# Kernel optimization log

Hardware: AMD Instinct MI355X
Metric: run time of the kernel (lower is better)

## Reference

```python
import jax, jax.numpy as jnp
import numpy as np

B, F, V, D, K = 16384, 39, 30000, 16, 20
EPS = 1e-5


def bn_eval(x, g, b):
    # inference-mode BatchNorm1d with running_mean=0, running_var=1
    return g * x / jnp.sqrt(1.0 + EPS) + b


def setup_inputs() -> dict:
    key = jax.random.key(0)
    ks = jax.random.split(key, 12)
    x = jax.random.randint(ks[0], (B, F), 0, V)
    emb_table = jax.random.normal(ks[1], (F * V, D), dtype=jnp.float32) * 0.05
    w_c = jax.random.normal(ks[2], (F, F * D), dtype=jnp.float32) * 0.05
    w0 = jax.random.normal(ks[3], (1024, F * D), dtype=jnp.float32) * 0.04
    w1 = jax.random.normal(ks[4], (512, 1024), dtype=jnp.float32) * 0.03
    w_out = jax.random.normal(ks[5], (1, 512), dtype=jnp.float32) * 0.04
    return {
        'x': x, 'emb_table': emb_table,
        'w_c': w_c, 'b_c': jnp.zeros((F,)), 'g_c': jnp.ones((F,)), 'be_c': jnp.zeros((F,)),
        'w0': w0, 'b0': jnp.zeros((1024,)), 'g0': jnp.ones((1024,)), 'be0': jnp.zeros((1024,)),
        'w1': w1, 'b1': jnp.zeros((512,)), 'g1': jnp.ones((512,)), 'be1': jnp.zeros((512,)),
        'w_out': w_out, 'b_out': jnp.zeros((1,)),
    }


def reference(x, emb_table, w_c, b_c, g_c, be_c, w0, b0, g0, be0,
              w1, b1, g1, be1, w_out, b_out):
    offsets = jnp.arange(F, dtype=x.dtype) * V          # per-field offsets
    idx = x + offsets[None, :]                          # [B, F]
    emb = emb_table[idx]                                # [B, F, D] gather

    # controller_mlp: flatten (batch, D, F) layout like torch transpose(1,2)
    flat = jnp.transpose(emb, (0, 2, 1)).reshape(B, F * D)
    h = jax.nn.relu(bn_eval(flat @ w_c.T + b_c, g_c, be_c))
    scores = jax.nn.softmax(h, axis=1)                  # [B, F]

    # kmax_pooling: top-k field indices, sorted ascending, gather weights
    _, kidx = jax.lax.top_k(scores, K)
    kidx = jnp.sort(kidx, axis=1)                       # [B, K]
    w = jnp.take_along_axis(scores, kidx, axis=1)       # [B, K]

    # forward_select: gather selected field embeddings, weight them
    sel = jnp.take_along_axis(emb, kidx[:, :, None], axis=1)  # [B, K, D]
    weighted = sel * w[:, :, None]

    # scatter back into full field slots (unselected fields are zero)
    full = jnp.zeros((B, F, D), weighted.dtype)
    bidx = jnp.arange(B)[:, None]
    full = full.at[bidx, kidx].set(weighted)            # [B, F, D]

    z = jnp.transpose(full, (0, 2, 1)).reshape(B, F * D)
    z = jax.nn.relu(bn_eval(z @ w0.T + b0, g0, be0))
    z = jax.nn.relu(bn_eval(z @ w1.T + b1, g1, be1))
    out = jax.nn.sigmoid(z @ w_out.T + b_out)           # [B, 1]
    return out.squeeze(-1)
```

## Files before the change

### kernel.cpp

```cpp
#include <hip/hip_runtime.h>
#include <math.h>

#define B_SZ 16384
#define F_N 39
#define V_N 30000
#define D_N 16
#define K_SEL 20
#define FD 624
#define KP0 640
#define NCP 48
#define N0 1024
#define N1 512
#define CBR 16
#define ALD 648

typedef unsigned short u16;
typedef __attribute__((ext_vector_type(8))) short bf16x8;
typedef __attribute__((ext_vector_type(8))) unsigned short u16x8;
typedef __attribute__((ext_vector_type(4))) float f32x4;
typedef __attribute__((ext_vector_type(4))) unsigned short u16x4;

__device__ __forceinline__ u16 f2bf(float v) {
    union { float f; unsigned u; } x; x.f = v;
    unsigned r = x.u + 0x7fff + ((x.u >> 16) & 1);
    return (u16)(r >> 16);
}
__device__ __forceinline__ float bf2f(u16 v) {
    union { unsigned u; float f; } x; x.u = ((unsigned)v) << 16;
    return x.f;
}

#define GLD16(gp, lp) __builtin_amdgcn_global_load_lds( \
    (const __attribute__((address_space(1))) unsigned int*)(gp), \
    (__attribute__((address_space(3))) unsigned int*)(lp), 16, 0, 0)

#define PREP_W0 (N0 * KP0)
#define PREP_W1 (N1 * N0)
#define PREP_WC (NCP * KP0)
#define PREP_TOT (PREP_W0 + PREP_W1 + PREP_WC + 3 * NCP)

__global__ __launch_bounds__(256) void prep_all_kernel(
    const float* __restrict__ w0, const float* __restrict__ w1,
    const float* __restrict__ w_c, const float* __restrict__ b_c,
    const float* __restrict__ g_c, const float* __restrict__ be_c,
    u16* __restrict__ w0b, u16* __restrict__ w1b, u16* __restrict__ wcb,
    float* __restrict__ bcp, float* __restrict__ gcp, float* __restrict__ becp)
{
    int i = blockIdx.x * blockDim.x + threadIdx.x;
    if (i < PREP_W0) {
        int n = i / KP0, kk = i - n * KP0;
        float v = 0.f;
        if (kk < FD) v = w0[n * FD + (kk & 15) * F_N + (kk >> 4)];
        w0b[i] = f2bf(v);
        return;
    }
    i -= PREP_W0;
    if (i < PREP_W1) { w1b[i] = f2bf(w1[i]); return; }
    i -= PREP_W1;
    if (i < PREP_WC) {
        int n = i / KP0, kk = i - n * KP0;
        float v = 0.f;
        if (n < F_N && kk < FD) v = w_c[n * FD + (kk & 15) * F_N + (kk >> 4)];
        wcb[i] = f2bf(v);
        return;
    }
    i -= PREP_WC;
    if (i < 3 * NCP) {
        int which = i / NCP, n = i - which * NCP;
        float v = 0.f;
        if (n < F_N) v = (which == 0) ? b_c[n] : (which == 1) ? g_c[n] : be_c[n];
        ((which == 0) ? bcp : (which == 1) ? gcp : becp)[n] = v;
    }
}

__global__ __launch_bounds__(256) void fused_controller_kernel(
    const int* __restrict__ x, const float* __restrict__ emb_table,
    const u16* __restrict__ wcb, const float* __restrict__ bcp,
    const float* __restrict__ gcp, const float* __restrict__ becp,
    u16* __restrict__ zb)
{
    __shared__ __align__(16) u16 Al[CBR * ALD];
    __shared__ float vv[CBR][49];
    __shared__ f32x4 part[4][64][3];
    __shared__ float selw[CBR][F_N];

    const int t    = threadIdx.x;
    const int wave = t >> 6;
    const int lane = t & 63;
    const int b0   = blockIdx.x * CBR;

    for (int p = t; p < CBR * F_N; p += 256) {
        const int row = p / F_N;
        const int f   = p - row * F_N;
        const int xi  = x[b0 * F_N + p];
        const float4* src = (const float4*)(emb_table + (size_t)(xi + f * V_N) * D_N);
        float4 v0 = src[0], v1 = src[1], v2 = src[2], v3 = src[3];
        u16x8 o0 = { f2bf(v0.x), f2bf(v0.y), f2bf(v0.z), f2bf(v0.w),
                     f2bf(v1.x), f2bf(v1.y), f2bf(v1.z), f2bf(v1.w) };
        u16x8 o1 = { f2bf(v2.x), f2bf(v2.y), f2bf(v2.z), f2bf(v2.w),
                     f2bf(v3.x), f2bf(v3.y), f2bf(v3.z), f2bf(v3.w) };
        *(u16x8*)&Al[row * ALD + f * D_N]     = o0;
        *(u16x8*)&Al[row * ALD + f * D_N + 8] = o1;
    }
    __syncthreads();

    const int m = lane & 15;
    const int q = lane >> 4;
    f32x4 acc0 = {}, acc1 = {}, acc2 = {};
    {
        const u16* ap  = &Al[m * ALD + wave * 160 + q * 8];
        const u16* bp0 = wcb + (size_t)(0  + m) * KP0 + wave * 160 + q * 8;
        const u16* bp1 = wcb + (size_t)(16 + m) * KP0 + wave * 160 + q * 8;
        const u16* bp2 = wcb + (size_t)(32 + m) * KP0 + wave * 160 + q * 8;
        #pragma unroll
        for (int k = 0; k < 5; ++k) {
            bf16x8 af = *(const bf16x8*)ap;
            bf16x8 b0 = *(const bf16x8*)bp0;
            bf16x8 b1 = *(const bf16x8*)bp1;
            bf16x8 b2 = *(const bf16x8*)bp2;
            acc0 = __builtin_amdgcn_mfma_f32_16x16x32_bf16(af, b0, acc0, 0, 0, 0);
            acc1 = __builtin_amdgcn_mfma_f32_16x16x32_bf16(af, b1, acc1, 0, 0, 0);
            acc2 = __builtin_amdgcn_mfma_f32_16x16x32_bf16(af, b2, acc2, 0, 0, 0);
            ap += 32; bp0 += 32; bp1 += 32; bp2 += 32;
        }
    }
    part[wave][lane][0] = acc0;
    part[wave][lane][1] = acc1;
    part[wave][lane][2] = acc2;
    __syncthreads();

    if (wave == 0) {
        f32x4 r0 = part[0][lane][0] + part[1][lane][0] + part[2][lane][0] + part[3][lane][0];
        f32x4 r1 = part[0][lane][1] + part[1][lane][1] + part[2][lane][1] + part[3][lane][1];
        f32x4 r2 = part[0][lane][2] + part[1][lane][2] + part[2][lane][2] + part[3][lane][2];

        const float rs = rsqrtf(1.0f + 1e-5f);
        #pragma unroll
        for (int j = 0; j < 3; ++j) {
            const f32x4 a = (j == 0) ? r0 : (j == 1) ? r1 : r2;
            const int n = j * 16 + m;
            const float gn = gcp[n] * rs;
            const float bn = becp[n];
            const float bi = bcp[n];
            #pragma unroll
            for (int r = 0; r < 4; ++r)
                vv[q * 4 + r][n] = fmaxf(fmaf(gn, a[r] + bi, bn), 0.f);
        }

        const int row = lane >> 2;
        const int fg  = lane & 3;
        float e[10];
        float mloc = -1e30f;
        #pragma unroll
        for (int it = 0; it < 10; ++it) {
            const int f = fg + 4 * it;
            if (f < F_N) { e[it] = vv[row][f]; mloc = fmaxf(mloc, e[it]); }
        }
        mloc = fmaxf(mloc, __shfl_xor(mloc, 1, 64));
        mloc = fmaxf(mloc, __shfl_xor(mloc, 2, 64));
        float sloc = 0.f;
        #pragma unroll
        for (int it = 0; it < 10; ++it) {
            const int f = fg + 4 * it;
            if (f < F_N) { e[it] = expf(e[it] - mloc); sloc += e[it]; }
        }
        sloc += __shfl_xor(sloc, 1, 64);
        sloc += __shfl_xor(sloc, 2, 64);
        const float inv = 1.f / sloc;
        #pragma unroll
        for (int it = 0; it < 10; ++it) {
            const int f = fg + 4 * it;
            if (f < F_N) vv[row][f] = e[it];
        }

        int rank[10] = {};
        for (int gg = 0; gg < F_N; ++gg) {
            const float o = vv[row][gg];
            #pragma unroll
            for (int it = 0; it < 10; ++it) {
                const int f = fg + 4 * it;
                if (f < F_N)
                    rank[it] += (o > e[it] || (o == e[it] && gg < f)) ? 1 : 0;
            }
        }
        #pragma unroll
        for (int it = 0; it < 10; ++it) {
            const int f = fg + 4 * it;
            if (f < F_N)
                selw[row][f] = (rank[it] < K_SEL) ? e[it] * inv : 0.f;
        }
    }
    __syncthreads();

    for (int gp = t; gp < CBR * 40; gp += 256) {
        const int row  = gp & 15;
        const int slot = gp >> 4;
        u16* dst = zb + (size_t)(b0 + row) * KP0 + slot * D_N;
        u16x8 o0 = {0,0,0,0,0,0,0,0}, o1 = {0,0,0,0,0,0,0,0};
        if (slot < F_N) {
            const float w = selw[row][slot];
            u16x8 a0 = *(u16x8*)&Al[row * ALD + slot * D_N];
            u16x8 a1 = *(u16x8*)&Al[row * ALD + slot * D_N + 8];
            #pragma unroll
            for (int k = 0; k < 8; ++k) {
                o0[k] = f2bf(bf2f(a0[k]) * w);
                o1[k] = f2bf(bf2f(a1[k]) * w);
            }
        }
        *(u16x8*)dst = o0;
        *(u16x8*)(dst + 8) = o1;
    }
}

template<int MODE>
__global__ __launch_bounds__(256) void gemm_mfma_bn_relu(
    const u16* __restrict__ A, const u16* __restrict__ W,
    const float* __restrict__ bias, const float* __restrict__ g,
    const float* __restrict__ be, u16* __restrict__ Cout,
    int M, int N, int Kp,
    const float* __restrict__ w_out, float* __restrict__ outp)
{
    __shared__ __align__(16) u16 As[128 * 32];
    __shared__ __align__(16) u16 Bs[128 * 32];

    const int t    = threadIdx.x;
    const int wave = t >> 6;
    const int lane = t & 63;
    const int wm   = wave >> 1, wn = wave & 1;
    const int m0   = blockIdx.x * 128;
    const int n0   = blockIdx.y * 128;

    const int lr    = lane >> 2;
    const int swz_u = (lane & 3) ^ ((lane >> 3) & 3);
    const u16* gA0 = A + (size_t)(m0 + wave * 32 + lr) * Kp + swz_u * 8;
    const u16* gA1 = gA0 + 16 * (size_t)Kp;
    const u16* gB0 = W + (size_t)(n0 + wave * 32 + lr) * Kp + swz_u * 8;
    const u16* gB1 = gB0 + 16 * (size_t)Kp;
    u16* lA0 = &As[(wave * 32)      * 32];
    u16* lA1 = &As[(wave * 32 + 16) * 32];
    u16* lB0 = &Bs[(wave * 32)      * 32];
    u16* lB1 = &Bs[(wave * 32 + 16) * 32];

    const int q    = lane >> 4;
    const int lr16 = lane & 15;

    int aoff[4], boff[4];
    #pragma unroll
    for (int i = 0; i < 4; ++i) {
        int ra = wm * 64 + i * 16 + lr16;
        aoff[i] = ra * 32 + ((q ^ ((ra >> 1) & 3)) * 8);
        int rb = wn * 64 + i * 16 + lr16;
        boff[i] = rb * 32 + ((q ^ ((rb >> 1) & 3)) * 8);
    }

    f32x4 acc[4][4] = {};

    for (int k0 = 0; k0 < Kp; k0 += 32) {
        GLD16(gA0, lA0); GLD16(gA1, lA1);
        GLD16(gB0, lB0); GLD16(gB1, lB1);
        gA0 += 32; gA1 += 32; gB0 += 32; gB1 += 32;
        __syncthreads();

        bf16x8 af[4], bfr[4];
        #pragma unroll
        for (int i = 0; i < 4; ++i) af[i]  = *(const bf16x8*)&As[aoff[i]];
        #pragma unroll
        for (int j = 0; j < 4; ++j) bfr[j] = *(const bf16x8*)&Bs[boff[j]];

        #pragma unroll
        for (int i = 0; i < 4; ++i)
            #pragma unroll
            for (int j = 0; j < 4; ++j)
                acc[i][j] = __builtin_amdgcn_mfma_f32_16x16x32_bf16(
                    af[i], bfr[j], acc[i][j], 0, 0, 0);
        __syncthreads();
    }

    const float rs = rsqrtf(1.0f + 1e-5f);
    if (MODE == 0) {
        #pragma unroll
        for (int j = 0; j < 4; ++j) {
            const int n = n0 + wn * 64 + j * 16 + lr16;
            const float bn_g = g[n] * rs;
            const float bn_b = be[n];
            const float bi   = bias[n];
            #pragma unroll
            for (int i = 0; i < 4; ++i) {
                const int mbase = m0 + wm * 64 + i * 16 + q * 4;
                #pragma unroll
                for (int r = 0; r < 4; ++r) {
                    float v = acc[i][j][r] + bi;
                    v = fmaxf(fmaf(bn_g, v, bn_b), 0.f);
                    Cout[(size_t)(mbase + r) * N + n] = f2bf(v);
                }
            }
        }
    } else {
        float s[4][4] = {};
        #pragma unroll
        for (int j = 0; j < 4; ++j) {
            const int n = n0 + wn * 64 + j * 16 + lr16;
            const float bn_g = g[n] * rs;
            const float bn_b = be[n];
            const float bi   = bias[n];
            const float wo   = w_out[n];
            #pragma unroll
            for (int i = 0; i < 4; ++i)
                #pragma unroll
                for (int r = 0; r < 4; ++r) {
                    float v = acc[i][j][r] + bi;
                    v = fmaxf(fmaf(bn_g, v, bn_b), 0.f);
                    s[i][r] = fmaf(v, wo, s[i][r]);
                }
        }
        #pragma unroll
        for (int i = 0; i < 4; ++i)
            #pragma unroll
            for (int r = 0; r < 4; ++r) {
                float v = s[i][r];
                v += __shfl_xor(v, 1, 64);
                v += __shfl_xor(v, 2, 64);
                v += __shfl_xor(v, 4, 64);
                v += __shfl_xor(v, 8, 64);
                s[i][r] = v;
            }
        if (lr16 == 0) {
            #pragma unroll
            for (int i = 0; i < 4; ++i) {
                const int mbase = m0 + wm * 64 + i * 16 + q * 4;
                #pragma unroll
                for (int r = 0; r < 4; ++r)
                    atomicAdd(&outp[mbase + r], s[i][r]);
            }
        }
    }
}

__global__ __launch_bounds__(256) void sigmoid_kernel(
    const float* __restrict__ outp, const float* __restrict__ b_out,
    float* __restrict__ out)
{
    const int b = blockIdx.x * 256 + threadIdx.x;
    out[b] = 1.f / (1.f + expf(-(outp[b] + b_out[0])));
}

extern "C" void kernel_launch(void* const* d_in, const int* in_sizes, int n_in,
                              void* d_out, int out_size, void* d_ws, size_t ws_size,
                              hipStream_t stream)
{
    const int*   x     = (const int*)  d_in[0];
    const float* emb   = (const float*)d_in[1];
    const float* w_c   = (const float*)d_in[2];
    const float* b_c   = (const float*)d_in[3];
    const float* g_c   = (const float*)d_in[4];
    const float* be_c  = (const float*)d_in[5];
    const float* w0    = (const float*)d_in[6];
    const float* b0    = (const float*)d_in[7];
    const float* g0    = (const float*)d_in[8];
    const float* be0   = (const float*)d_in[9];
    const float* w1    = (const float*)d_in[10];
    const float* b1    = (const float*)d_in[11];
    const float* g1    = (const float*)d_in[12];
    const float* be1   = (const float*)d_in[13];
    const float* w_out = (const float*)d_in[14];
    const float* b_out = (const float*)d_in[15];
    float* out = (float*)d_out;

    u16*   zb    = (u16*)d_ws;
    u16*   w0b   = zb    + (size_t)B_SZ * KP0;
    u16*   h0b   = w0b   + (size_t)N0 * KP0;
    u16*   w1b   = h0b   + (size_t)B_SZ * N0;
    u16*   wcb   = w1b   + (size_t)N1 * N0;
    float* outp  = (float*)(wcb + (size_t)NCP * KP0);
    float* bcp   = outp + B_SZ;
    float* gcp   = bcp + NCP;
    float* becp  = gcp + NCP;

    prep_all_kernel<<<(PREP_TOT + 255) / 256, 256, 0, stream>>>(
        w0, w1, w_c, b_c, g_c, be_c, w0b, w1b, wcb, bcp, gcp, becp);

    fused_controller_kernel<<<B_SZ / CBR, 256, 0, stream>>>(
        x, emb, wcb, bcp, gcp, becp, zb);

    gemm_mfma_bn_relu<0><<<dim3(B_SZ / 128, N0 / 128), 256, 0, stream>>>(
        zb, w0b, b0, g0, be0, h0b, B_SZ, N0, KP0, nullptr, nullptr);

    hipMemsetAsync(outp, 0, B_SZ * sizeof(float), stream);

    gemm_mfma_bn_relu<1><<<dim3(B_SZ / 128, N1 / 128), 256, 0, stream>>>(
        h0b, w1b, b1, g1, be1, nullptr, B_SZ, N1, N0, w_out, outp);

    sigmoid_kernel<<<B_SZ / 256, 256, 0, stream>>>(outp, b_out, out);
}
```

Measured before the change: 230.7 us.

## Double-buffer GEMM LDS tiles and spread controller softmax/top-k across all waves

The main GEMM now keeps two LDS buffers, issuing the next tile's global-to-LDS loads before computing on the current one, with one barrier per k-step instead of two. This is meant to overlap global memory latency with MFMA work, at the cost of twice the LDS use per block, which can lower occupancy. The controller kernel also splits the BN/ReLU, softmax and rank-based top-k across all four waves (16 lanes per row) instead of only wave 0. That adds one barrier there but cuts serial per-lane work.

Measured after the change: 223.3 us. 1.03x faster.

```diff
diff --git a/kernel.cpp b/kernel.cpp
--- a/kernel.cpp
+++ b/kernel.cpp
@@ -129,63 +129,72 @@
     part[wave][lane][2] = acc2;
     __syncthreads();
 
-    if (wave == 0) {
+    {
         f32x4 r0 = part[0][lane][0] + part[1][lane][0] + part[2][lane][0] + part[3][lane][0];
         f32x4 r1 = part[0][lane][1] + part[1][lane][1] + part[2][lane][1] + part[3][lane][1];
         f32x4 r2 = part[0][lane][2] + part[1][lane][2] + part[2][lane][2] + part[3][lane][2];
 
         const float rs = rsqrtf(1.0f + 1e-5f);
-        #pragma unroll
-        for (int j = 0; j < 3; ++j) {
-            const f32x4 a = (j == 0) ? r0 : (j == 1) ? r1 : r2;
-            const int n = j * 16 + m;
-            const float gn = gcp[n] * rs;
-            const float bn = becp[n];
-            const float bi = bcp[n];
-            #pragma unroll
-            for (int r = 0; r < 4; ++r)
-                vv[q * 4 + r][n] = fmaxf(fmaf(gn, a[r] + bi, bn), 0.f);
-        }
-
-        const int row = lane >> 2;
-        const int fg  = lane & 3;
-        float e[10];
+        if (q == wave) {
+            #pragma unroll
+            for (int j = 0; j < 3; ++j) {
+                const f32x4 a = (j == 0) ? r0 : (j == 1) ? r1 : r2;
+                const int n = j * 16 + m;
+                const float gn = gcp[n] * rs;
+                const float bn = becp[n];
+                const float bi = bcp[n];
+                #pragma unroll
+                for (int r = 0; r < 4; ++r)
+                    vv[wave * 4 + r][n] = fmaxf(fmaf(gn, a[r] + bi, bn), 0.f);
+            }
+        }
+    }
+    __syncthreads();
+
+    {
+        const int row = wave * 4 + (lane >> 4);
+        const int fl  = lane & 15;
+        float e[3] = {0.f, 0.f, 0.f};
         float mloc = -1e30f;
         #pragma unroll
-        for (int it = 0; it < 10; ++it) {
-            const int f = fg + 4 * it;
+        for (int it = 0; it < 3; ++it) {
+            const int f = fl + 16 * it;
             if (f < F_N) { e[it] = vv[row][f]; mloc = fmaxf(mloc, e[it]); }
         }
         mloc = fmaxf(mloc, __shfl_xor(mloc, 1, 64));
         mloc = fmaxf(mloc, __shfl_xor(mloc, 2, 64));
+        mloc = fmaxf(mloc, __shfl_xor(mloc, 4, 64));
+        mloc = fmaxf(mloc, __shfl_xor(mloc, 8, 64));
         float sloc = 0.f;
         #pragma unroll
-        for (int it = 0; it < 10; ++it) {
-            const int f = fg + 4 * it;
+        for (int it = 0; it < 3; ++it) {
+            const int f = fl + 16 * it;
             if (f < F_N) { e[it] = expf(e[it] - mloc); sloc += e[it]; }
         }
         sloc += __shfl_xor(sloc, 1, 64);
         sloc += __shfl_xor(sloc, 2, 64);
+        sloc += __shfl_xor(sloc, 4, 64);
+        sloc += __shfl_xor(sloc, 8, 64);
         const float inv = 1.f / sloc;
         #pragma unroll
-        for (int it = 0; it < 10; ++it) {
-            const int f = fg + 4 * it;
+        for (int it = 0; it < 3; ++it) {
+            const int f = fl + 16 * it;
             if (f < F_N) vv[row][f] = e[it];
         }
 
-        int rank[10] = {};
+        int rank[3] = {};
         for (int gg = 0; gg < F_N; ++gg) {
             const float o = vv[row][gg];
             #pragma unroll
-            for (int it = 0; it < 10; ++it) {
-                const int f = fg + 4 * it;
+            for (int it = 0; it < 3; ++it) {
+                const int f = fl + 16 * it;
                 if (f < F_N)
                     rank[it] += (o > e[it] || (o == e[it] && gg < f)) ? 1 : 0;
             }
         }
         #pragma unroll
-        for (int it = 0; it < 10; ++it) {
-            const int f = fg + 4 * it;
+        for (int it = 0; it < 3; ++it) {
+            const int f = fl + 16 * it;
             if (f < F_N)
                 selw[row][f] = (rank[it] < K_SEL) ? e[it] * inv : 0.f;
         }
@@ -220,8 +229,8 @@
     int M, int N, int Kp,
     const float* __restrict__ w_out, float* __restrict__ outp)
 {
-    __shared__ __align__(16) u16 As[128 * 32];
-    __shared__ __align__(16) u16 Bs[128 * 32];
+    __shared__ __align__(16) u16 As[2][128 * 32];
+    __shared__ __align__(16) u16 Bs[2][128 * 32];
 
     const int t    = threadIdx.x;
     const int wave = t >> 6;
@@ -233,13 +242,10 @@
     const int lr    = lane >> 2;
     const int swz_u = (lane & 3) ^ ((lane >> 3) & 3);
     const u16* gA0 = A + (size_t)(m0 + wave * 32 + lr) * Kp + swz_u * 8;
-    const u16* gA1 = gA0 + 16 * (size_t)Kp;
     const u16* gB0 = W + (size_t)(n0 + wave * 32 + lr) * Kp + swz_u * 8;
-    const u16* gB1 = gB0 + 16 * (size_t)Kp;
-    u16* lA0 = &As[(wave * 32)      * 32];
-    u16* lA1 = &As[(wave * 32 + 16) * 32];
-    u16* lB0 = &Bs[(wave * 32)      * 32];
-    u16* lB1 = &Bs[(wave * 32 + 16) * 32];
+    const size_t kstep16 = 16 * (size_t)Kp;
+    const int oA0 = (wave * 32) * 32;
+    const int oA1 = (wave * 32 + 16) * 32;
 
     const int q    = lane >> 4;
     const int lr16 = lane & 15;
@@ -253,19 +259,30 @@
         boff[i] = rb * 32 + ((q ^ ((rb >> 1) & 3)) * 8);
     }
 
+    GLD16(gA0,           &As[0][oA0]);
+    GLD16(gA0 + kstep16, &As[0][oA1]);
+    GLD16(gB0,           &Bs[0][oA0]);
+    GLD16(gB0 + kstep16, &Bs[0][oA1]);
+    gA0 += 32; gB0 += 32;
+
     f32x4 acc[4][4] = {};
+    int buf = 0;
 
     for (int k0 = 0; k0 < Kp; k0 += 32) {
-        GLD16(gA0, lA0); GLD16(gA1, lA1);
-        GLD16(gB0, lB0); GLD16(gB1, lB1);
-        gA0 += 32; gA1 += 32; gB0 += 32; gB1 += 32;
         __syncthreads();
+        if (k0 + 32 < Kp) {
+            GLD16(gA0,           &As[buf ^ 1][oA0]);
+            GLD16(gA0 + kstep16, &As[buf ^ 1][oA1]);
+            GLD16(gB0,           &Bs[buf ^ 1][oA0]);
+            GLD16(gB0 + kstep16, &Bs[buf ^ 1][oA1]);
+            gA0 += 32; gB0 += 32;
+        }
 
         bf16x8 af[4], bfr[4];
         #pragma unroll
-        for (int i = 0; i < 4; ++i) af[i]  = *(const bf16x8*)&As[aoff[i]];
-        #pragma unroll
-        for (int j = 0; j < 4; ++j) bfr[j] = *(const bf16x8*)&Bs[boff[j]];
+        for (int i = 0; i < 4; ++i) af[i]  = *(const bf16x8*)&As[buf][aoff[i]];
+        #pragma unroll
+        for (int j = 0; j < 4; ++j) bfr[j] = *(const bf16x8*)&Bs[buf][boff[j]];
 
         #pragma unroll
         for (int i = 0; i < 4; ++i)
@@ -273,7 +290,7 @@
             for (int j = 0; j < 4; ++j)
                 acc[i][j] = __builtin_amdgcn_mfma_f32_16x16x32_bf16(
                     af[i], bfr[j], acc[i][j], 0, 0, 0);
-        __syncthreads();
+        buf ^= 1;
     }
 
     const float rs = rsqrtf(1.0f + 1e-5f);
```
